# Optimization experiments

Hardware: AMD Instinct MI355X
Metric: run time of the kernel (lower is better)

## Reference

```python
import jax, jax.numpy as jnp
import numpy as np

N, E, F_IN, HEADS, PER_HEAD, CLS = 50000, 800000, 256, 8, 32, 40  # per_head = ceil(256/8)
TOTAL_HIDDEN = HEADS * PER_HEAD  # 256


def setup_inputs() -> dict:
    key = jax.random.key(0)
    ks = jax.random.split(key, 12)
    s = 0.1
    x = jax.random.normal(ks[0], (N, F_IN), jnp.float32)
    edge_index = jax.random.randint(ks[1], (2, E), 0, N, dtype=jnp.int32)
    W1 = jax.random.normal(ks[2], (F_IN, TOTAL_HIDDEN), jnp.float32) * s
    att_src1 = jax.random.normal(ks[3], (HEADS, PER_HEAD), jnp.float32) * s
    att_dst1 = jax.random.normal(ks[4], (HEADS, PER_HEAD), jnp.float32) * s
    b1 = jnp.zeros((TOTAL_HIDDEN,), jnp.float32)
    gamma = jnp.ones((TOTAL_HIDDEN,), jnp.float32)
    beta = jnp.zeros((TOTAL_HIDDEN,), jnp.float32)
    W2 = jax.random.normal(ks[5], (TOTAL_HIDDEN, CLS), jnp.float32) * s
    att_src2 = jax.random.normal(ks[6], (1, CLS), jnp.float32) * s
    att_dst2 = jax.random.normal(ks[7], (1, CLS), jnp.float32) * s
    b2 = jnp.zeros((CLS,), jnp.float32)
    return dict(x=x, edge_index=edge_index, W1=W1, att_src1=att_src1, att_dst1=att_dst1,
                b1=b1, gamma=gamma, beta=beta, W2=W2, att_src2=att_src2, att_dst2=att_dst2, b2=b2)


def gat_layer(x, edge_index, W, a_src, a_dst, bias, concat):
    """PyG GATConv (add_self_loops=True, negative_slope=0.2, eval-mode dropout)."""
    n = x.shape[0]
    heads, ch = a_src.shape
    loop = jnp.arange(n, dtype=edge_index.dtype)
    src = jnp.concatenate([edge_index[0], loop])  # message source j
    dst = jnp.concatenate([edge_index[1], loop])  # message destination i
    h = (x @ W).reshape(n, heads, ch)                       # [N,H,C]
    alpha_src = jnp.sum(h * a_src, axis=-1)                 # [N,H]
    alpha_dst = jnp.sum(h * a_dst, axis=-1)                 # [N,H]
    e = jax.nn.leaky_relu(alpha_src[src] + alpha_dst[dst], 0.2)  # [E',H]
    # segment softmax over incoming edges of each dst node (self-loops ensure non-empty segments)
    m = jax.ops.segment_max(e, dst, num_segments=n)
    p = jnp.exp(e - m[dst])
    denom = jax.ops.segment_sum(p, dst, num_segments=n)
    alpha = p / (denom[dst] + 1e-16)                        # [E',H]
    out = jax.ops.segment_sum(alpha[:, :, None] * h[src], dst, num_segments=n)  # [N,H,C]
    out = out.reshape(n, heads * ch) if concat else out.mean(axis=1)
    return out + bias


def reference(x, edge_index, W1, att_src1, att_dst1, b1, gamma, beta, W2, att_src2, att_dst2, b2):
    h = gat_layer(x, edge_index, W1, att_src1, att_dst1, b1, concat=True)   # [N, 256]
    # BatchNorm1d (training-mode batch statistics, eps=1e-5)
    mu = h.mean(axis=0)
    var = h.var(axis=0)
    h = (h - mu) / jnp.sqrt(var + 1e-5) * gamma + beta
    h = jax.nn.elu(h)
    return gat_layer(h, edge_index, W2, att_src2, att_dst2, b2, concat=False)  # [N, CLS]
```

## Files before the change

### kernel.cpp

```cpp
#include <hip/hip_runtime.h>
#include <hip/hip_bf16.h>
#include <hip/hip_fp16.h>

#define THREADS 256

typedef __attribute__((ext_vector_type(8))) short short8;
typedef __attribute__((ext_vector_type(4))) float f32x4;

__device__ inline unsigned short f2bf_rn(float f) {
    unsigned u = __float_as_uint(f);
    unsigned r = (u + 0x7FFF + ((u >> 16) & 1)) >> 16;
    return (unsigned short)r;
}
__device__ inline float bf2f(unsigned short s) {
    return __uint_as_float(((unsigned)s) << 16);
}
__device__ inline void bfsplit(float f, short* hi, short* lo) {
    unsigned short h = f2bf_rn(f);
    *hi = (short)h;
    *lo = (short)f2bf_rn(f - bf2f(h));
}


__global__ void k_count(const int* __restrict__ dstv, int E, int* __restrict__ deg) {
    int e = blockIdx.x * THREADS + threadIdx.x;
    if (e < E) atomicAdd(&deg[dstv[e]], 1);
}

__global__ void k_scanA(const int* __restrict__ deg, int* __restrict__ partial, int Nn) {
    __shared__ int sm[256];
    int i = blockIdx.x * 256 + threadIdx.x;
    sm[threadIdx.x] = (i < Nn) ? deg[i] + 1 : 0;
    __syncthreads();
    for (int off = 128; off > 0; off >>= 1) {
        if (threadIdx.x < off) sm[threadIdx.x] += sm[threadIdx.x + off];
        __syncthreads();
    }
    if (threadIdx.x == 0) partial[blockIdx.x] = sm[0];
}

__global__ void k_scanB(const int* __restrict__ partial, int* __restrict__ partoff,
                        int* __restrict__ rowptr, int nb, int Nn) {
    __shared__ int sm[256];
    int t = threadIdx.x;
    int v = (t < nb) ? partial[t] : 0;
    sm[t] = v;
    __syncthreads();
    for (int off = 1; off < 256; off <<= 1) {
        int u = (t >= off) ? sm[t - off] : 0;
        __syncthreads();
        sm[t] += u;
        __syncthreads();
    }
    if (t < nb) partoff[t] = sm[t] - v;
    if (t == 255) rowptr[Nn] = sm[255];
}

__global__ void k_scanC(int* __restrict__ deg_cursor, const int* __restrict__ partoff,
                        int* __restrict__ rowptr, int* __restrict__ colx, int Nn) {
    __shared__ int sm[256];
    int t = threadIdx.x;
    int i = blockIdx.x * 256 + t;
    int d = (i < Nn) ? deg_cursor[i] : 0;
    int v = (i < Nn) ? d + 1 : 0;
    sm[t] = v;
    __syncthreads();
    for (int off = 1; off < 256; off <<= 1) {
        int u = (t >= off) ? sm[t - off] : 0;
        __syncthreads();
        sm[t] += u;
        __syncthreads();
    }
    int excl = sm[t] - v + partoff[blockIdx.x];
    if (i < Nn) {
        rowptr[i] = excl;
        colx[excl] = i;
        deg_cursor[i] = excl + 1;
    }
}

__global__ void k_scatter(const int* __restrict__ srcv, const int* __restrict__ dstv,
                          int E, int* __restrict__ cursor, int* __restrict__ colx) {
    int e = blockIdx.x * THREADS + threadIdx.x;
    if (e >= E) return;
    int pos = atomicAdd(&cursor[dstv[e]], 1);
    colx[pos] = srcv[e];
}


__global__ void k_packW1(const float* __restrict__ W, short* __restrict__ Wh,
                         short* __restrict__ Wl) {
    int g = blockIdx.x * 256 + threadIdx.x;
    int col = g >> 5, k8 = (g & 31) * 8;
    short8 h, l;
    #pragma unroll
    for (int i = 0; i < 8; ++i) {
        short hh, ll;
        bfsplit(W[(size_t)(k8 + i) * 256 + col], &hh, &ll);
        h[i] = hh; l[i] = ll;
    }
    *(short8*)&Wh[col * 256 + k8] = h;
    *(short8*)&Wl[col * 256 + k8] = l;
}

__global__ void k_packW2(const float* __restrict__ W, short* __restrict__ Wh,
                         short* __restrict__ Wl) {
    int g = blockIdx.x * 256 + threadIdx.x;
    int col = g >> 5, k8 = (g & 31) * 8;
    short8 h, l;
    #pragma unroll
    for (int i = 0; i < 8; ++i) {
        short hh = 0, ll = 0;
        if (col < 40) bfsplit(W[(size_t)(k8 + i) * 40 + col], &hh, &ll);
        h[i] = hh; l[i] = ll;
    }
    *(short8*)&Wh[col * 256 + k8] = h;
    *(short8*)&Wl[col * 256 + k8] = l;
}


__global__ __launch_bounds__(512) void k_gemm1(const float* __restrict__ A,
                                               const short* __restrict__ W1h,
                                               const short* __restrict__ W1l,
                                               const float* __restrict__ attS,
                                               const float* __restrict__ attD,
                                               __half* __restrict__ C,
                                               float* __restrict__ as1,
                                               float* __restrict__ ad1, int M) {
    __shared__ short Ash[64][40];
    __shared__ short Asl[64][40];
    int t = threadIdx.x;
    int l = t & 63, wc = t >> 6;
    int row0 = blockIdx.x * 64;
    int l16 = l & 15, lg = l >> 4;

    f32x4 zero = {0.f, 0.f, 0.f, 0.f};
    f32x4 acc[4][2];
    #pragma unroll
    for (int i = 0; i < 4; ++i) { acc[i][0] = zero; acc[i][1] = zero; }

    for (int k0 = 0; k0 < 256; k0 += 32) {
        {
            int r = t >> 3, c4 = t & 7;
            int grow = row0 + r;
            float4 v = {0.f, 0.f, 0.f, 0.f};
            if (grow < M) v = *(const float4*)&A[(size_t)grow * 256 + k0 + c4 * 4];
            short h, lo2;
            bfsplit(v.x, &h, &lo2); Ash[r][c4 * 4 + 0] = h; Asl[r][c4 * 4 + 0] = lo2;
            bfsplit(v.y, &h, &lo2); Ash[r][c4 * 4 + 1] = h; Asl[r][c4 * 4 + 1] = lo2;
            bfsplit(v.z, &h, &lo2); Ash[r][c4 * 4 + 2] = h; Asl[r][c4 * 4 + 2] = lo2;
            bfsplit(v.w, &h, &lo2); Ash[r][c4 * 4 + 3] = h; Asl[r][c4 * 4 + 3] = lo2;
        }
        short8 bh[2], bl[2];
        #pragma unroll
        for (int nf = 0; nf < 2; ++nf) {
            int col = wc * 32 + nf * 16 + l16;
            bh[nf] = *(const short8*)&W1h[col * 256 + k0 + lg * 8];
            bl[nf] = *(const short8*)&W1l[col * 256 + k0 + lg * 8];
        }
        __syncthreads();
        #pragma unroll
        for (int mf = 0; mf < 4; ++mf) {
            short8 ah = *(const short8*)&Ash[mf * 16 + l16][lg * 8];
            short8 al = *(const short8*)&Asl[mf * 16 + l16][lg * 8];
            #pragma unroll
            for (int nf = 0; nf < 2; ++nf) {
                acc[mf][nf] = __builtin_amdgcn_mfma_f32_16x16x32_bf16(ah, bh[nf], acc[mf][nf], 0, 0, 0);
                acc[mf][nf] = __builtin_amdgcn_mfma_f32_16x16x32_bf16(ah, bl[nf], acc[mf][nf], 0, 0, 0);
                acc[mf][nf] = __builtin_amdgcn_mfma_f32_16x16x32_bf16(al, bh[nf], acc[mf][nf], 0, 0, 0);
            }
        }
        __syncthreads();
    }

    #pragma unroll
    for (int mf = 0; mf < 4; ++mf)
        #pragma unroll
        for (int nf = 0; nf < 2; ++nf)
            #pragma unroll
            for (int j = 0; j < 4; ++j) {
                int row = row0 + mf * 16 + 4 * lg + j;
                if (row < M)
                    C[(size_t)row * 256 + wc * 32 + nf * 16 + l16] =
                        __float2half(acc[mf][nf][j]);
            }

    {
        float aS0 = attS[wc * 32 + l16],      aD0 = attD[wc * 32 + l16];
        float aS1 = attS[wc * 32 + 16 + l16], aD1 = attD[wc * 32 + 16 + l16];
        #pragma unroll
        for (int mf = 0; mf < 4; ++mf) {
            float ps[4], pd[4];
            #pragma unroll
            for (int j = 0; j < 4; ++j) {
                ps[j] = acc[mf][0][j] * aS0 + acc[mf][1][j] * aS1;
                pd[j] = acc[mf][0][j] * aD0 + acc[mf][1][j] * aD1;
            }
            #pragma unroll
            for (int msk = 1; msk < 16; msk <<= 1)
                #pragma unroll
                for (int j = 0; j < 4; ++j) {
                    ps[j] += __shfl_xor(ps[j], msk);
                    pd[j] += __shfl_xor(pd[j], msk);
                }
            if (l16 == 0) {
                #pragma unroll
                for (int j = 0; j < 4; ++j) {
                    int row = row0 + mf * 16 + 4 * lg + j;
                    if (row < M) {
                        as1[row * 8 + wc] = ps[j];
                        ad1[row * 8 + wc] = pd[j];
                    }
                }
            }
        }
    }
}


__global__ __launch_bounds__(256) void k_agg1(const __half* __restrict__ h1,
                                              const float* __restrict__ as1,
                                              const float* __restrict__ ad1,
                                              const int* __restrict__ rowptr,
                                              const int* __restrict__ colx,
                                              const float* __restrict__ b1,
                                              float* __restrict__ hb, int Nn) {
    int lane = threadIdx.x & 63, w = threadIdx.x >> 6;
    int n = blockIdx.x * 4 + w;
    if (n >= Nn) return;
    int head = lane >> 3;
    float ad = ad1[n * 8 + head];
    int beg = rowptr[n], end = rowptr[n + 1];
    float m = -1e30f, s = 0.f;
    float acc[4] = {};
    int i = beg;
    for (; i + 3 < end; i += 4) {
        int s0 = colx[i], s1 = colx[i + 1], s2 = colx[i + 2], s3 = colx[i + 3];
        uint2 r0 = *(const uint2*)&h1[(size_t)s0 * 256 + lane * 4];
        uint2 r1 = *(const uint2*)&h1[(size_t)s1 * 256 + lane * 4];
        uint2 r2 = *(const uint2*)&h1[(size_t)s2 * 256 + lane * 4];
        uint2 r3 = *(const uint2*)&h1[(size_t)s3 * 256 + lane * 4];
        float e0 = as1[s0 * 8 + head] + ad;
        float e1 = as1[s1 * 8 + head] + ad;
        float e2 = as1[s2 * 8 + head] + ad;
        float e3 = as1[s3 * 8 + head] + ad;
        e0 = e0 > 0.f ? e0 : 0.2f * e0;
        e1 = e1 > 0.f ? e1 : 0.2f * e1;
        e2 = e2 > 0.f ? e2 : 0.2f * e2;
        e3 = e3 > 0.f ? e3 : 0.2f * e3;
        float nm = fmaxf(fmaxf(m, fmaxf(e0, e1)), fmaxf(e2, e3));
        float r  = __expf(m - nm);
        float p0 = __expf(e0 - nm), p1 = __expf(e1 - nm);
        float p2 = __expf(e2 - nm), p3 = __expf(e3 - nm);
        float2 f00 = __half22float2(*(__half2*)&r0.x), f01 = __half22float2(*(__half2*)&r0.y);
        float2 f10 = __half22float2(*(__half2*)&r1.x), f11 = __half22float2(*(__half2*)&r1.y);
        float2 f20 = __half22float2(*(__half2*)&r2.x), f21 = __half22float2(*(__half2*)&r2.y);
        float2 f30 = __half22float2(*(__half2*)&r3.x), f31 = __half22float2(*(__half2*)&r3.y);
        float hv0[4] = {f00.x, f00.y, f01.x, f01.y};
        float hv1[4] = {f10.x, f10.y, f11.x, f11.y};
        float hv2[4] = {f20.x, f20.y, f21.x, f21.y};
        float hv3[4] = {f30.x, f30.y, f31.x, f31.y};
        s = s * r + (p0 + p1) + (p2 + p3);
        #pragma unroll
        for (int q = 0; q < 4; ++q)
            acc[q] = acc[q] * r + (p0 * hv0[q] + p1 * hv1[q]) + (p2 * hv2[q] + p3 * hv3[q]);
        m = nm;
    }
    for (; i < end; ++i) {
        int s0 = colx[i];
        uint2 raw = *(const uint2*)&h1[(size_t)s0 * 256 + lane * 4];
        float e = as1[s0 * 8 + head] + ad;
        e = e > 0.f ? e : 0.2f * e;
        float nm = fmaxf(m, e);
        float r = __expf(m - nm);
        float p = __expf(e - nm);
        float2 f0 = __half22float2(*(__half2*)&raw.x);
        float2 f1 = __half22float2(*(__half2*)&raw.y);
        float hv[4] = {f0.x, f0.y, f1.x, f1.y};
        s = s * r + p;
        #pragma unroll
        for (int q = 0; q < 4; ++q) acc[q] = acc[q] * r + p * hv[q];
        m = nm;
    }
    float inv = 1.f / (s + 1e-16f);
    float4 bv = *(const float4*)&b1[lane * 4];
    float4 o = {acc[0] * inv + bv.x, acc[1] * inv + bv.y,
                acc[2] * inv + bv.z, acc[3] * inv + bv.w};
    *(float4*)&hb[(size_t)n * 256 + lane * 4] = o;
}


__global__ __launch_bounds__(256) void k_bnstats(const float* __restrict__ hb,
                                                 float* __restrict__ bnsum,
                                                 float* __restrict__ bnssum, int Nn) {
    int c = threadIdx.x;
    float s = 0.f, ss = 0.f;
    for (int r = blockIdx.x; r < Nn; r += gridDim.x) {
        float v = hb[(size_t)r * 256 + c];
        s += v; ss += v * v;
    }
    atomicAdd(&bnsum[c], s);
    atomicAdd(&bnssum[c], ss);
}

__global__ void k_bnfinal(const float* __restrict__ bnsum, const float* __restrict__ bnssum,
                          const float* __restrict__ gamma, const float* __restrict__ beta,
                          float* __restrict__ scale, float* __restrict__ shift, int Nn) {
    int c = threadIdx.x;
    float mu = bnsum[c] / (float)Nn;
    float var = bnssum[c] / (float)Nn - mu * mu;
    float inv = rsqrtf(var + 1e-5f);
    float sc = gamma[c] * inv;
    scale[c] = sc;
    shift[c] = beta[c] - mu * sc;
}


__global__ __launch_bounds__(256) void k_gemm2(const float* __restrict__ H,
                                               const short* __restrict__ W2h,
                                               const short* __restrict__ W2l,
                                               const float* __restrict__ scale,
                                               const float* __restrict__ shift,
                                               __half* __restrict__ h2, int M) {
    __shared__ short Ash[64][40];
    __shared__ short Asl[64][40];
    __shared__ float ssc[256], ssh[256];
    int t = threadIdx.x;
    ssc[t] = scale[t];
    ssh[t] = shift[t];
    int l = t & 63, wc = t >> 6;
    int row0 = blockIdx.x * 64;
    int l16 = l & 15, lg = l >> 4;

    f32x4 zero = {0.f, 0.f, 0.f, 0.f};
    f32x4 acc[4];
    #pragma unroll
    for (int i = 0; i < 4; ++i) acc[i] = zero;
    __syncthreads();

    for (int k0 = 0; k0 < 256; k0 += 32) {
        #pragma unroll
        for (int p = 0; p < 2; ++p) {
            int s = t + p * 256;
            int r = s >> 3, c4 = s & 7;
            int grow = row0 + r;
            float4 v = {0.f, 0.f, 0.f, 0.f};
            if (grow < M) v = *(const float4*)&H[(size_t)grow * 256 + k0 + c4 * 4];
            int c = k0 + c4 * 4;
            float e0 = v.x * ssc[c + 0] + ssh[c + 0];
            float e1 = v.y * ssc[c + 1] + ssh[c + 1];
            float e2 = v.z * ssc[c + 2] + ssh[c + 2];
            float e3 = v.w * ssc[c + 3] + ssh[c + 3];
            e0 = e0 > 0.f ? e0 : __expf(e0) - 1.f;
            e1 = e1 > 0.f ? e1 : __expf(e1) - 1.f;
            e2 = e2 > 0.f ? e2 : __expf(e2) - 1.f;
            e3 = e3 > 0.f ? e3 : __expf(e3) - 1.f;
            short h, lo2;
            bfsplit(e0, &h, &lo2); Ash[r][c4 * 4 + 0] = h; Asl[r][c4 * 4 + 0] = lo2;
            bfsplit(e1, &h, &lo2); Ash[r][c4 * 4 + 1] = h; Asl[r][c4 * 4 + 1] = lo2;
            bfsplit(e2, &h, &lo2); Ash[r][c4 * 4 + 2] = h; Asl[r][c4 * 4 + 2] = lo2;
            bfsplit(e3, &h, &lo2); Ash[r][c4 * 4 + 3] = h; Asl[r][c4 * 4 + 3] = lo2;
        }
        short8 bh, bl;
        {
            int col = wc * 16 + l16;
            bh = *(const short8*)&W2h[col * 256 + k0 + lg * 8];
            bl = *(const short8*)&W2l[col * 256 + k0 + lg * 8];
        }
        __syncthreads();
        #pragma unroll
        for (int mf = 0; mf < 4; ++mf) {
            short8 ah = *(const short8*)&Ash[mf * 16 + l16][lg * 8];
            short8 al = *(const short8*)&Asl[mf * 16 + l16][lg * 8];
            acc[mf] = __builtin_amdgcn_mfma_f32_16x16x32_bf16(ah, bh, acc[mf], 0, 0, 0);
            acc[mf] = __builtin_amdgcn_mfma_f32_16x16x32_bf16(ah, bl, acc[mf], 0, 0, 0);
            acc[mf] = __builtin_amdgcn_mfma_f32_16x16x32_bf16(al, bh, acc[mf], 0, 0, 0);
        }
        __syncthreads();
    }

    int col = wc * 16 + l16;
    #pragma unroll
    for (int mf = 0; mf < 4; ++mf)
        #pragma unroll
        for (int j = 0; j < 4; ++j) {
            int row = row0 + mf * 16 + 4 * lg + j;
            if (row < M && col < 40)
                h2[(size_t)row * 40 + col] = __float2half(acc[mf][j]);
        }
}


__global__ void k_alpha2(const __half* __restrict__ h2, const float* __restrict__ atts,
                         const float* __restrict__ attd, float* __restrict__ as2,
                         float* __restrict__ ad2, int Nn) {
    int n = blockIdx.x * THREADS + threadIdx.x;
    if (n >= Nn) return;
    const __half2* hp = (const __half2*)&h2[(size_t)n * 40];
    float s = 0.f, d = 0.f;
    #pragma unroll
    for (int j = 0; j < 20; ++j) {
        float2 v = __half22float2(hp[j]);
        s += v.x * atts[2 * j] + v.y * atts[2 * j + 1];
        d += v.x * attd[2 * j] + v.y * attd[2 * j + 1];
    }
    as2[n] = s; ad2[n] = d;
}


__global__ __launch_bounds__(256) void k_agg2(const __half* __restrict__ h2,
                                              const float* __restrict__ as2,
                                              const float* __restrict__ ad2,
                                              const int* __restrict__ rowptr,
                                              const int* __restrict__ colx,
                                              const float* __restrict__ b2,
                                              float* __restrict__ out, int Nn) {
    int lane = threadIdx.x & 63, w = threadIdx.x >> 6;
    int n = blockIdx.x * 4 + w;
    if (n >= Nn) return;
    float ad = ad2[n];
    int beg = rowptr[n], end = rowptr[n + 1];
    int c = lane < 40 ? lane : 0;
    float m = -1e30f, s = 0.f, acc = 0.f;
    int i = beg;
    for (; i + 3 < end; i += 4) {
        int s0 = colx[i], s1 = colx[i + 1], s2 = colx[i + 2], s3 = colx[i + 3];
        float h0 = __half2float(h2[(size_t)s0 * 40 + c]);
        float h1v = __half2float(h2[(size_t)s1 * 40 + c]);
        float h2v = __half2float(h2[(size_t)s2 * 40 + c]);
        float h3 = __half2float(h2[(size_t)s3 * 40 + c]);
        float e0 = as2[s0] + ad, e1 = as2[s1] + ad;
        float e2 = as2[s2] + ad, e3 = as2[s3] + ad;
        e0 = e0 > 0.f ? e0 : 0.2f * e0;
        e1 = e1 > 0.f ? e1 : 0.2f * e1;
        e2 = e2 > 0.f ? e2 : 0.2f * e2;
        e3 = e3 > 0.f ? e3 : 0.2f * e3;
        float nm = fmaxf(fmaxf(m, fmaxf(e0, e1)), fmaxf(e2, e3));
        float r  = __expf(m - nm);
        float p0 = __expf(e0 - nm), p1 = __expf(e1 - nm);
        float p2 = __expf(e2 - nm), p3 = __expf(e3 - nm);
        s = s * r + (p0 + p1) + (p2 + p3);
        acc = acc * r + (p0 * h0 + p1 * h1v) + (p2 * h2v + p3 * h3);
        m = nm;
    }
    for (; i < end; ++i) {
        int s0 = colx[i];
        float hv = __half2float(h2[(size_t)s0 * 40 + c]);
        float e = as2[s0] + ad;
        e = e > 0.f ? e : 0.2f * e;
        float nm = fmaxf(m, e);
        float r = __expf(m - nm);
        float p = __expf(e - nm);
        s = s * r + p;
        acc = acc * r + p * hv;
        m = nm;
    }
    if (lane < 40) out[(size_t)n * 40 + lane] = acc / (s + 1e-16f) + b2[lane];
}


static inline size_t rup(size_t x) { return (x + 255) & ~(size_t)255; }

extern "C" void kernel_launch(void* const* d_in, const int* in_sizes, int n_in,
                              void* d_out, int out_size, void* d_ws, size_t ws_size,
                              hipStream_t stream) {
    const float* x     = (const float*)d_in[0];
    const int*   ei    = (const int*)d_in[1];
    const float* W1    = (const float*)d_in[2];
    const float* atts1 = (const float*)d_in[3];
    const float* attd1 = (const float*)d_in[4];
    const float* b1    = (const float*)d_in[5];
    const float* gamma = (const float*)d_in[6];
    const float* beta  = (const float*)d_in[7];
    const float* W2    = (const float*)d_in[8];
    const float* atts2 = (const float*)d_in[9];
    const float* attd2 = (const float*)d_in[10];
    const float* b2    = (const float*)d_in[11];

    const int N = in_sizes[0] / 256;
    const int E = in_sizes[1] / 2;
    const int* srcv = ei;
    const int* dstv = ei + E;

    char* w = (char*)d_ws;
    __half* h1 = (__half*)w;    w += rup((size_t)N * 256 * 2);
    float* hb = (float*)w;      w += rup((size_t)N * 256 * 4);
    __half* h2 = (__half*)w;    w += rup((size_t)N * 40 * 2);
    float* as1 = (float*)w;     w += rup((size_t)N * 8 * 4);
    float* ad1 = (float*)w;     w += rup((size_t)N * 8 * 4);
    float* as2 = (float*)w;     w += rup((size_t)N * 4);
    float* ad2 = (float*)w;     w += rup((size_t)N * 4);
    int* rowptr = (int*)w;      w += rup((size_t)(N + 1) * 4);
    int* cursor = (int*)w;      w += rup((size_t)N * 4);
    int* colx = (int*)w;        w += rup((size_t)(E + N) * 4);
    int* partial = (int*)w;     w += rup(256 * 4);
    int* partoff = (int*)w;     w += rup(256 * 4);
    float* bn = (float*)w;      w += rup(1024 * 4);
    float* bnsum = bn, *bnssum = bn + 256, *scale = bn + 512, *shift = bn + 768;
    short* W1h = (short*)w;     w += rup(256 * 256 * 2);
    short* W1l = (short*)w;     w += rup(256 * 256 * 2);
    short* W2h = (short*)w;     w += rup(64 * 256 * 2);
    short* W2l = (short*)w;     w += rup(64 * 256 * 2);

    const int NB = (N + 255) / 256;

    k_packW1<<<32, 256, 0, stream>>>(W1, W1h, W1l);
    k_packW2<<<8, 256, 0, stream>>>(W2, W2h, W2l);

    hipMemsetAsync(cursor, 0, (size_t)N * 4, stream);
    hipMemsetAsync(bn, 0, 512 * 4, stream);
    k_count<<<(E + THREADS - 1) / THREADS, THREADS, 0, stream>>>(dstv, E, cursor);
    k_scanA<<<NB, 256, 0, stream>>>(cursor, partial, N);
    k_scanB<<<1, 256, 0, stream>>>(partial, partoff, rowptr, NB, N);
    k_scanC<<<NB, 256, 0, stream>>>(cursor, partoff, rowptr, colx, N);
    k_scatter<<<(E + THREADS - 1) / THREADS, THREADS, 0, stream>>>(srcv, dstv, E, cursor, colx);

    k_gemm1<<<(N + 63) / 64, 512, 0, stream>>>(x, W1h, W1l, atts1, attd1, h1, as1, ad1, N);
    k_agg1<<<(N + 3) / 4, 256, 0, stream>>>(h1, as1, ad1, rowptr, colx, b1, hb, N);

    k_bnstats<<<512, 256, 0, stream>>>(hb, bnsum, bnssum, N);
    k_bnfinal<<<1, 256, 0, stream>>>(bnsum, bnssum, gamma, beta, scale, shift, N);

    k_gemm2<<<(N + 63) / 64, 256, 0, stream>>>(hb, W2h, W2l, scale, shift, h2, N);
    k_alpha2<<<(N + THREADS - 1) / THREADS, THREADS, 0, stream>>>(h2, atts2, attd2, as2, ad2, N);
    k_agg2<<<(N + 3) / 4, 256, 0, stream>>>(h2, as2, ad2, rowptr, colx, b2, (float*)d_out, N);
}
```

Before: 411.2 us.

## Drop A-low bf16 split in GEMMs, store layer-1 output in fp16, use exp2

Both GEMMs stop splitting the activation operand into hi/lo bf16 parts, which removes one of the three MFMAs per tile and the second shared-memory buffer. The layer-1 aggregated output hb is stored as fp16 instead of fp32, halving the traffic for the BN stats and GEMM2 reads. Attention logits are prescaled by log2(e) so the softmax can use exp2f. The cost is lower precision in the activations and GEMM inputs, which may add accuracy error.

```diff
diff --git a/kernel.cpp b/kernel.cpp
--- a/kernel.cpp
+++ b/kernel.cpp
@@ -3,6 +3,7 @@
 #include <hip/hip_fp16.h>
 
 #define THREADS 256
+#define LOG2E 1.44269504f
 
 typedef __attribute__((ext_vector_type(8))) short short8;
 typedef __attribute__((ext_vector_type(4))) float f32x4;
@@ -128,7 +129,6 @@
                                                float* __restrict__ as1,
                                                float* __restrict__ ad1, int M) {
     __shared__ short Ash[64][40];
-    __shared__ short Asl[64][40];
     int t = threadIdx.x;
     int l = t & 63, wc = t >> 6;
     int row0 = blockIdx.x * 64;
@@ -145,11 +145,10 @@
             int grow = row0 + r;
             float4 v = {0.f, 0.f, 0.f, 0.f};
             if (grow < M) v = *(const float4*)&A[(size_t)grow * 256 + k0 + c4 * 4];
-            short h, lo2;
-            bfsplit(v.x, &h, &lo2); Ash[r][c4 * 4 + 0] = h; Asl[r][c4 * 4 + 0] = lo2;
-            bfsplit(v.y, &h, &lo2); Ash[r][c4 * 4 + 1] = h; Asl[r][c4 * 4 + 1] = lo2;
-            bfsplit(v.z, &h, &lo2); Ash[r][c4 * 4 + 2] = h; Asl[r][c4 * 4 + 2] = lo2;
-            bfsplit(v.w, &h, &lo2); Ash[r][c4 * 4 + 3] = h; Asl[r][c4 * 4 + 3] = lo2;
+            Ash[r][c4 * 4 + 0] = (short)f2bf_rn(v.x);
+            Ash[r][c4 * 4 + 1] = (short)f2bf_rn(v.y);
+            Ash[r][c4 * 4 + 2] = (short)f2bf_rn(v.z);
+            Ash[r][c4 * 4 + 3] = (short)f2bf_rn(v.w);
         }
         short8 bh[2], bl[2];
         #pragma unroll
@@ -162,12 +161,10 @@
         #pragma unroll
         for (int mf = 0; mf < 4; ++mf) {
             short8 ah = *(const short8*)&Ash[mf * 16 + l16][lg * 8];
-            short8 al = *(const short8*)&Asl[mf * 16 + l16][lg * 8];
             #pragma unroll
             for (int nf = 0; nf < 2; ++nf) {
                 acc[mf][nf] = __builtin_amdgcn_mfma_f32_16x16x32_bf16(ah, bh[nf], acc[mf][nf], 0, 0, 0);
                 acc[mf][nf] = __builtin_amdgcn_mfma_f32_16x16x32_bf16(ah, bl[nf], acc[mf][nf], 0, 0, 0);
-                acc[mf][nf] = __builtin_amdgcn_mfma_f32_16x16x32_bf16(al, bh[nf], acc[mf][nf], 0, 0, 0);
             }
         }
         __syncthreads();
@@ -208,8 +205,8 @@
                 for (int j = 0; j < 4; ++j) {
                     int row = row0 + mf * 16 + 4 * lg + j;
                     if (row < M) {
-                        as1[row * 8 + wc] = ps[j];
-                        ad1[row * 8 + wc] = pd[j];
+                        as1[row * 8 + wc] = ps[j] * LOG2E;
+                        ad1[row * 8 + wc] = pd[j] * LOG2E;
                     }
                 }
             }
@@ -224,7 +221,7 @@
                                               const int* __restrict__ rowptr,
                                               const int* __restrict__ colx,
                                               const float* __restrict__ b1,
-                                              float* __restrict__ hb, int Nn) {
+                                              __half* __restrict__ hb, int Nn) {
     int lane = threadIdx.x & 63, w = threadIdx.x >> 6;
     int n = blockIdx.x * 4 + w;
     if (n >= Nn) return;
@@ -249,9 +246,9 @@
         e2 = e2 > 0.f ? e2 : 0.2f * e2;
         e3 = e3 > 0.f ? e3 : 0.2f * e3;
         float nm = fmaxf(fmaxf(m, fmaxf(e0, e1)), fmaxf(e2, e3));
-        float r  = __expf(m - nm);
-        float p0 = __expf(e0 - nm), p1 = __expf(e1 - nm);
-        float p2 = __expf(e2 - nm), p3 = __expf(e3 - nm);
+        float r  = exp2f(m - nm);
+        float p0 = exp2f(e0 - nm), p1 = exp2f(e1 - nm);
+        float p2 = exp2f(e2 - nm), p3 = exp2f(e3 - nm);
         float2 f00 = __half22float2(*(__half2*)&r0.x), f01 = __half22float2(*(__half2*)&r0.y);
         float2 f10 = __half22float2(*(__half2*)&r1.x), f11 = __half22float2(*(__half2*)&r1.y);
         float2 f20 = __half22float2(*(__half2*)&r2.x), f21 = __half22float2(*(__half2*)&r2.y);
@@ -272,8 +269,8 @@
         float e = as1[s0 * 8 + head] + ad;
         e = e > 0.f ? e : 0.2f * e;
         float nm = fmaxf(m, e);
-        float r = __expf(m - nm);
-        float p = __expf(e - nm);
+        float r = exp2f(m - nm);
+        float p = exp2f(e - nm);
         float2 f0 = __half22float2(*(__half2*)&raw.x);
         float2 f1 = __half22float2(*(__half2*)&raw.y);
         float hv[4] = {f0.x, f0.y, f1.x, f1.y};
@@ -284,19 +281,22 @@
     }
     float inv = 1.f / (s + 1e-16f);
     float4 bv = *(const float4*)&b1[lane * 4];
-    float4 o = {acc[0] * inv + bv.x, acc[1] * inv + bv.y,
-                acc[2] * inv + bv.z, acc[3] * inv + bv.w};
-    *(float4*)&hb[(size_t)n * 256 + lane * 4] = o;
-}
-
-
-__global__ __launch_bounds__(256) void k_bnstats(const float* __restrict__ hb,
+    __half2 o01 = __floats2half2_rn(acc[0] * inv + bv.x, acc[1] * inv + bv.y);
+    __half2 o23 = __floats2half2_rn(acc[2] * inv + bv.z, acc[3] * inv + bv.w);
+    uint2 ow;
+    ow.x = *(unsigned*)&o01;
+    ow.y = *(unsigned*)&o23;
+    *(uint2*)&hb[(size_t)n * 256 + lane * 4] = ow;
+}
+
+
+__global__ __launch_bounds__(256) void k_bnstats(const __half* __restrict__ hb,
                                                  float* __restrict__ bnsum,
                                                  float* __restrict__ bnssum, int Nn) {
     int c = threadIdx.x;
     float s = 0.f, ss = 0.f;
     for (int r = blockIdx.x; r < Nn; r += gridDim.x) {
-        float v = hb[(size_t)r * 256 + c];
+        float v = __half2float(hb[(size_t)r * 256 + c]);
         s += v; ss += v * v;
     }
     atomicAdd(&bnsum[c], s);
@@ -316,14 +316,13 @@
 }
 
 
-__global__ __launch_bounds__(256) void k_gemm2(const float* __restrict__ H,
+__global__ __launch_bounds__(256) void k_gemm2(const __half* __restrict__ H,
                                                const short* __restrict__ W2h,
                                                const short* __restrict__ W2l,
                                                const float* __restrict__ scale,
                                                const float* __restrict__ shift,
                                                __half* __restrict__ h2, int M) {
     __shared__ short Ash[64][40];
-    __shared__ short Asl[64][40];
     __shared__ float ssc[256], ssh[256];
     int t = threadIdx.x;
     ssc[t] = scale[t];
@@ -344,22 +343,23 @@
             int s = t + p * 256;
             int r = s >> 3, c4 = s & 7;
             int grow = row0 + r;
-            float4 v = {0.f, 0.f, 0.f, 0.f};
-            if (grow < M) v = *(const float4*)&H[(size_t)grow * 256 + k0 + c4 * 4];
+            uint2 raw = {0u, 0u};
+            if (grow < M) raw = *(const uint2*)&H[(size_t)grow * 256 + k0 + c4 * 4];
+            float2 f0 = __half22float2(*(__half2*)&raw.x);
+            float2 f1 = __half22float2(*(__half2*)&raw.y);
             int c = k0 + c4 * 4;
-            float e0 = v.x * ssc[c + 0] + ssh[c + 0];
-            float e1 = v.y * ssc[c + 1] + ssh[c + 1];
-            float e2 = v.z * ssc[c + 2] + ssh[c + 2];
-            float e3 = v.w * ssc[c + 3] + ssh[c + 3];
+            float e0 = f0.x * ssc[c + 0] + ssh[c + 0];
+            float e1 = f0.y * ssc[c + 1] + ssh[c + 1];
+            float e2 = f1.x * ssc[c + 2] + ssh[c + 2];
+            float e3 = f1.y * ssc[c + 3] + ssh[c + 3];
             e0 = e0 > 0.f ? e0 : __expf(e0) - 1.f;
             e1 = e1 > 0.f ? e1 : __expf(e1) - 1.f;
             e2 = e2 > 0.f ? e2 : __expf(e2) - 1.f;
             e3 = e3 > 0.f ? e3 : __expf(e3) - 1.f;
-            short h, lo2;
-            bfsplit(e0, &h, &lo2); Ash[r][c4 * 4 + 0] = h; Asl[r][c4 * 4 + 0] = lo2;
-            bfsplit(e1, &h, &lo2); Ash[r][c4 * 4 + 1] = h; Asl[r][c4 * 4 + 1] = lo2;
-            bfsplit(e2, &h, &lo2); Ash[r][c4 * 4 + 2] = h; Asl[r][c4 * 4 + 2] = lo2;
-            bfsplit(e3, &h, &lo2); Ash[r][c4 * 4 + 3] = h; Asl[r][c4 * 4 + 3] = lo2;
+            Ash[r][c4 * 4 + 0] = (short)f2bf_rn(e0);
+            Ash[r][c4 * 4 + 1] = (short)f2bf_rn(e1);
+            Ash[r][c4 * 4 + 2] = (short)f2bf_rn(e2);
+            Ash[r][c4 * 4 + 3] = (short)f2bf_rn(e3);
         }
         short8 bh, bl;
         {
@@ -371,10 +371,8 @@
         #pragma unroll
         for (int mf = 0; mf < 4; ++mf) {
             short8 ah = *(const short8*)&Ash[mf * 16 + l16][lg * 8];
-            short8 al = *(const short8*)&Asl[mf * 16 + l16][lg * 8];
             acc[mf] = __builtin_amdgcn_mfma_f32_16x16x32_bf16(ah, bh, acc[mf], 0, 0, 0);
             acc[mf] = __builtin_amdgcn_mfma_f32_16x16x32_bf16(ah, bl, acc[mf], 0, 0, 0);
-            acc[mf] = __builtin_amdgcn_mfma_f32_16x16x32_bf16(al, bh, acc[mf], 0, 0, 0);
         }
         __syncthreads();
     }
@@ -404,7 +402,8 @@
         s += v.x * atts[2 * j] + v.y * atts[2 * j + 1];
         d += v.x * attd[2 * j] + v.y * attd[2 * j + 1];
     }
-    as2[n] = s; ad2[n] = d;
+    as2[n] = s * LOG2E;
+    ad2[n] = d * LOG2E;
 }
 
 
@@ -436,9 +435,9 @@
         e2 = e2 > 0.f ? e2 : 0.2f * e2;
         e3 = e3 > 0.f ? e3 : 0.2f * e3;
         float nm = fmaxf(fmaxf(m, fmaxf(e0, e1)), fmaxf(e2, e3));
-        float r  = __expf(m - nm);
-        float p0 = __expf(e0 - nm), p1 = __expf(e1 - nm);
-        float p2 = __expf(e2 - nm), p3 = __expf(e3 - nm);
+        float r  = exp2f(m - nm);
+        float p0 = exp2f(e0 - nm), p1 = exp2f(e1 - nm);
+        float p2 = exp2f(e2 - nm), p3 = exp2f(e3 - nm);
         s = s * r + (p0 + p1) + (p2 + p3);
         acc = acc * r + (p0 * h0 + p1 * h1v) + (p2 * h2v + p3 * h3);
         m = nm;
@@ -449,8 +448,8 @@
         float e = as2[s0] + ad;
         e = e > 0.f ? e : 0.2f * e;
         float nm = fmaxf(m, e);
-        float r = __expf(m - nm);
-        float p = __expf(e - nm);
+        float r = exp2f(m - nm);
+        float p = exp2f(e - nm);
         s = s * r + p;
         acc = acc * r + p * hv;
         m = nm;
@@ -484,7 +483,7 @@
 
     char* w = (char*)d_ws;
     __half* h1 = (__half*)w;    w += rup((size_t)N * 256 * 2);
-    float* hb = (float*)w;      w += rup((size_t)N * 256 * 4);
+    __half* hb = (__half*)w;    w += rup((size_t)N * 256 * 2);
     __half* h2 = (__half*)w;    w += rup((size_t)N * 40 * 2);
     float* as1 = (float*)w;     w += rup((size_t)N * 8 * 4);
     float* ad1 = (float*)w;     w += rup((size_t)N * 8 * 4);
```

New measurement: 409.0 us. No clear change (-0.5%).
